# Kernel optimization log

Measured on AMD Instinct MI355X. Metric: run time of the kernel, lower is better.

The kernel has to match this reference:

```python
import jax, jax.numpy as jnp
import numpy as np
from jax import lax

EPS = 1e-5
TAU = 2.0
THR = 1.0

@jax.custom_vjp
def spike_fn(x):
    # torch.heaviside(x, 1.0): 1 where x >= 0, else 0
    return (x >= 0).astype(x.dtype)

def _spike_fwd(x):
    return spike_fn(x), x

def _spike_bwd(x, g):
    alpha = 4.0
    s = jax.nn.sigmoid(alpha * x)
    return (g * (1.0 - s) * s * alpha,)

spike_fn.defvjp(_spike_fwd, _spike_bwd)

def lif(x):
    # sequential membrane recurrence over dim 0 (time)
    def step(v, xt):
        v = v + (xt - v) / TAU
        s = spike_fn(v - THR)
        v = (1.0 - lax.stop_gradient(s)) * v
        return v, s
    _, spikes = lax.scan(step, jnp.zeros_like(x[0]), x)
    return spikes

def bn(x, p):
    # eval-mode BatchNorm2d; p = [weight, bias, mean, var], each [C]
    w, b, m, v = p
    inv = w / jnp.sqrt(v + EPS)
    return (x - m[None, :, None, None]) * inv[None, :, None, None] + b[None, :, None, None]

def bn_and_pad(x, p):
    # BN then pad 1 pixel on all sides with the BN-of-zero value
    w, b, m, v = p
    y = bn(x, p)
    pad_val = b - m * w / jnp.sqrt(v + EPS)  # [C]
    y = jnp.pad(y, ((0, 0), (0, 0), (1, 1), (1, 1)))
    pv = pad_val[None, :, None]  # broadcasts over batch and spatial
    y = y.at[:, :, 0, :].set(pv)
    y = y.at[:, :, -1, :].set(pv)
    y = y.at[:, :, :, 0].set(pv)
    y = y.at[:, :, :, -1].set(pv)
    return y

def branch(x, w1, dw, pw, bn3):
    # RepConv: 1x1 -> BNAndPad(1) -> depthwise3x3(valid) -> 1x1 -> BN, then outer BN
    C = x.shape[1]
    y = jnp.einsum('oc,bchw->bohw', w1, x)
    y = bn_and_pad(y, bn3[0])
    y = lax.conv_general_dilated(y, dw[:, None, :, :], (1, 1), 'VALID',
                                 dimension_numbers=('NCHW', 'OIHW', 'NCHW'),
                                 feature_group_count=C)
    y = jnp.einsum('oc,bchw->bohw', pw, y)
    y = bn(y, bn3[1])
    y = bn(y, bn3[2])
    return y

def _to_heads(t, B, N, h, d):
    # [B,C,H,W] -> [B,h,N,d]
    return t.reshape(B, h * d, N).transpose(0, 2, 1).reshape(B, N, h, d).transpose(0, 2, 1, 3)

def forward(x, q_w1, q_dw, q_pw, q_bn, k_w1, k_dw, k_pw, k_bn,
            v_w1, v_dw, v_pw, v_bn, p_w1, p_dw, p_pw, p_bn,
            num_heads=8):
    B, C, H, W = x.shape
    N = H * W
    h = num_heads
    d = C // h
    scale = float(d) ** -0.5

    xs = lif(x)
    q = lif(branch(xs, q_w1, q_dw, q_pw, q_bn))
    k = lif(branch(xs, k_w1, k_dw, k_pw, k_bn))
    v = lif(branch(xs, v_w1, v_dw, v_pw, v_bn))

    q = _to_heads(q, B, N, h, d)
    k = _to_heads(k, B, N, h, d)
    v = _to_heads(v, B, N, h, d)

    kv = jnp.einsum('bhnd,bhne->bhde', k, v)          # [B,h,d,d]
    o = jnp.einsum('bhnd,bhde->bhne', q, kv) * scale  # [B,h,N,d]
    o = o.transpose(0, 1, 3, 2).reshape(B, C, N)       # [B,C,N]
    o = lif(o)
    o = o.reshape(B, C, H, W)
    o = branch(o, p_w1, p_dw, p_pw, p_bn)
    return o.reshape(B, C, H, W)

def setup_inputs() -> dict:
    key = jax.random.key(0)
    ks = jax.random.split(key, 20)
    B, C, H, W = 8, 256, 64, 64
    s1 = 1.0 / np.sqrt(C)

    def make_bn(k):
        k1, k2, k3, k4 = jax.random.split(k, 4)
        w = 1.0 + 0.1 * jax.random.normal(k1, (3, C), jnp.float32)
        b = 0.1 * jax.random.normal(k2, (3, C), jnp.float32)
        m = 0.1 * jax.random.normal(k3, (3, C), jnp.float32)
        var = jax.random.uniform(k4, (3, C), jnp.float32, 0.5, 1.5)
        return jnp.stack([w, b, m, var], axis=1)  # [3,4,C]

    inp = {'x': jax.random.normal(ks[0], (B, C, H, W), jnp.float32)}
    for i, p in enumerate(['q', 'k', 'v', 'p']):
        kk = jax.random.split(ks[1 + i], 4)
        inp[p + '_w1'] = jax.random.normal(kk[0], (C, C), jnp.float32) * s1
        inp[p + '_dw'] = jax.random.normal(kk[1], (C, 3, 3), jnp.float32) * 0.3
        inp[p + '_pw'] = jax.random.normal(kk[2], (C, C), jnp.float32) * s1
        inp[p + '_bn'] = make_bn(kk[3])
    return inp

def reference(x, q_w1, q_dw, q_pw, q_bn, k_w1, k_dw, k_pw, k_bn,
              v_w1, v_dw, v_pw, v_bn, p_w1, p_dw, p_pw, p_bn):
    return forward(x, q_w1, q_dw, q_pw, q_bn, k_w1, k_dw, k_pw, k_bn,
                   v_w1, v_dw, v_pw, v_bn, p_w1, p_dw, p_pw, p_bn)
```

## Files before the change

kernel.cpp:

```cpp
#include <hip/hip_runtime.h>
#include <hip/hip_bf16.h>
#include <math.h>

#define T_ 8
#define C_ 256
#define N_ 4096
#define CN_ (C_ * N_)
#define EPSB 1e-5f

typedef unsigned long long u64;
typedef unsigned int u32;
typedef short bf16x8 __attribute__((ext_vector_type(8)));
typedef float f32x4 __attribute__((ext_vector_type(4)));

static __device__ __forceinline__ unsigned short f2bf(float f) {
    __hip_bfloat16 h = __float2bfloat16(f);
    return *(unsigned short*)&h;
}
static __device__ __forceinline__ float bf2f(unsigned short u) {
    u32 x = (u32)u << 16;
    return *(float*)&x;
}

typedef const __attribute__((address_space(1))) unsigned int ga_u32;
typedef __attribute__((address_space(3))) unsigned int la_u32;
static __device__ __forceinline__ void gl_lds16(const unsigned short* g,
                                                unsigned short* l_) {
    __builtin_amdgcn_global_load_lds((ga_u32*)g, (la_u32*)l_, 16, 0, 0);
}


__global__ __launch_bounds__(256) void lif_x_frag(const float* __restrict__ X,
                                                  unsigned short* __restrict__ ST) {
    int nb = blockIdx.x * 32;
    int c0 = blockIdx.y * 8;
    int tid = threadIdx.x;
    int nj = tid & 31, ci = tid >> 5;
    size_t base = (size_t)(c0 + ci) * N_ + nb + nj;
    __shared__ unsigned short Ls[8][34];
    int k32 = c0 >> 5, quad = (c0 >> 3) & 3;
    float v = 0.f;
#pragma unroll
    for (int t = 0; t < T_; t++) {
        float xt = X[(size_t)t * CN_ + base];
        v = v + (xt - v) / 2.0f;
        int s = (v - 1.0f >= 0.f) ? 1 : 0;
        Ls[ci][nj] = s ? (unsigned short)0x3F80 : (unsigned short)0;
        if (s) v = 0.f;
        __syncthreads();
        if (tid < 32) {
            int np = nb + tid;
            bf16x8 bs;
#pragma unroll
            for (int j = 0; j < 8; j++) bs[j] = (short)Ls[j][tid];
            *(bf16x8*)&ST[(size_t)t * CN_ +
                ((size_t)((np >> 4) * 8 + k32)) * 512 + (quad * 16 + (np & 15)) * 8] = bs;
        }
        __syncthreads();
    }
}

struct LArgs {
    const float* F[3];
    unsigned char* sq;
    u64* kbp;
    u64* vbp;
};
__global__ __launch_bounds__(256) void lif3(LArgs a) {
    int br = blockIdx.y;
    int idx = blockIdx.x * 256 + threadIdx.x;
    const float* X = a.F[br];
    int lane = threadIdx.x & 63;
    u64* BP = (br == 1) ? a.kbp : a.vbp;
    float v = 0.f;
#pragma unroll
    for (int t = 0; t < T_; t++) {
        float xt = X[(size_t)t * CN_ + idx];
        v = v + (xt - v) / 2.0f;
        int s = (v - 1.0f >= 0.f) ? 1 : 0;
        if (br == 0) {
            a.sq[(size_t)t * CN_ + idx] = (unsigned char)s;
        } else {
            u64 mask = __ballot(s);
            if (lane == 0) BP[((size_t)t * CN_ + idx) >> 6] = mask;
        }
        if (s) v = 0.f;
    }
}

struct WPtrs { const float* w[8]; };
__global__ __launch_bounds__(256) void split_w(WPtrs p, unsigned short* __restrict__ out) {
    int mat = blockIdx.y;
    int idx = blockIdx.x * 256 + threadIdx.x;
    int m = idx >> 8, k = idx & 255;
    float w = p.w[mat][idx];
    unsigned short h1 = f2bf(w);
    float f1 = bf2f(h1);
    unsigned short h2 = f2bf(w - f1);
    unsigned short h3 = f2bf(w - f1 - bf2f(h2));
    int lane = ((k >> 3) & 3) * 16 + (m & 15);
    size_t pos = ((size_t)(((m >> 4) * 8 + (k >> 5)) * 64 + lane)) * 8 + (k & 7);
    size_t base = (size_t)mat * 3 * 65536;
    out[base + pos] = h1;
    out[base + 65536 + pos] = h2;
    out[base + 2 * 65536 + pos] = h3;
}

static __device__ __forceinline__ void dw_body(const float* __restrict__ Yt,
                                               const float* __restrict__ dw,
                                               const float* __restrict__ bnp,
                                               unsigned short* __restrict__ Bh,
                                               unsigned short* __restrict__ Bl,
                                               int y0, int cg, int tid) {
    int c0 = cg * 8;
    __shared__ float L[8][6][68];
    __shared__ float invs[8], bs_[8], ms_[8], pads_[8];

    if (tid < 8) {
        int c = c0 + tid;
        float w = bnp[c], b = bnp[256 + c], m = bnp[512 + c], var = bnp[768 + c];
        float sq = sqrtf(var + EPSB);
        invs[tid] = w / sq;
        bs_[tid] = b;
        ms_[tid] = m;
        pads_[tid] = b - (m * w) / sq;
    }
    __syncthreads();

    for (int i = tid; i < 8 * 6 * 66; i += 256) {
        int c = i / 396;
        int rem = i - c * 396;
        int row = rem / 66, col = rem - row * 66;
        int gy = y0 - 1 + row, gx = col - 1;
        float val;
        if (gy < 0 || gy > 63 || gx < 0 || gx > 63) val = pads_[c];
        else val = (Yt[(size_t)(c0 + c) * N_ + gy * 64 + gx] - ms_[c]) * invs[c] + bs_[c];
        L[c][row][col] = val;
    }
    __syncthreads();

    int x = tid & 63, ry = tid >> 6;
    int n = (y0 + ry) * 64 + x;

    bf16x8 hi, lo;
#pragma unroll
    for (int j = 0; j < 8; j++) {
        const float* dwc = dw + (c0 + j) * 9;
        float a = 0.f;
#pragma unroll
        for (int dy = 0; dy < 3; dy++)
#pragma unroll
            for (int dx = 0; dx < 3; dx++)
                a += dwc[dy * 3 + dx] * L[j][ry + dy][x + dx];
        unsigned short h = f2bf(a);
        hi[j] = (short)h;
        lo[j] = (short)f2bf(a - bf2f(h));
    }
    size_t pos = ((size_t)((n >> 4) * 8 + (cg >> 2))) * 512 +
                 (size_t)(((cg & 3) * 16 + (n & 15)) * 8);
    *(bf16x8*)&Bh[pos] = hi;
    *(bf16x8*)&Bl[pos] = lo;
}

__global__ __launch_bounds__(256) void dw_bn_split(const float* __restrict__ Yin,
                                                   const float* __restrict__ dw,
                                                   const float* __restrict__ bnp,
                                                   unsigned short* __restrict__ BhT,
                                                   unsigned short* __restrict__ BlT) {
    int t = blockIdx.z;
    dw_body(Yin + (size_t)t * CN_, dw, bnp,
            BhT + (size_t)t * CN_, BlT + (size_t)t * CN_,
            blockIdx.x * 4, blockIdx.y, threadIdx.x);
}

struct DArgs {
    const float* F[3];
    const float* dw[3];
    const float* bn[3];
    unsigned short* Ph[3];
    unsigned short* Pl[3];
};
__global__ __launch_bounds__(256) void dw3(DArgs a) {
    int br = blockIdx.z >> 3, t = blockIdx.z & 7;
    dw_body(a.F[br] + (size_t)t * CN_, a.dw[br], a.bn[br],
            a.Ph[br] + (size_t)t * CN_, a.Pl[br] + (size_t)t * CN_,
            blockIdx.x * 4, blockIdx.y, threadIdx.x);
}

static __device__ __forceinline__ void gemm_s_core(const unsigned short* __restrict__ Wsp,
                                                   const unsigned short* __restrict__ Bt,
                                                   float* __restrict__ Yt,
                                                   int bx, int by, int tid) {
    int l = tid & 63, wave = tid >> 6;
    int wm = wave >> 1, wn = wave & 1;
    int lcol = l & 15, quad = l >> 4;

    __shared__ unsigned short As[24][512];
    __shared__ unsigned short Bs[8][512];

    f32x4 acc[4][4];
#pragma unroll
    for (int i = 0; i < 4; i++)
#pragma unroll
        for (int j = 0; j < 4; j++) acc[i][j] = (f32x4){0.f, 0.f, 0.f, 0.f};

    for (int k32 = 0; k32 < 8; k32++) {
#pragma unroll
        for (int i = 0; i < 8; i++) {
            int tau = wave * 8 + i;
            if (tau < 24) {
                int s = tau >> 3, mtg = tau & 7;
                gl_lds16(&Wsp[(size_t)s * 65536 +
                              ((size_t)((by * 8 + mtg) * 8 + k32)) * 512 + l * 8],
                         &As[tau][0]);
            } else {
                int nt = tau - 24;
                gl_lds16(&Bt[((size_t)((bx * 8 + nt) * 8 + k32)) * 512 + l * 8],
                         &Bs[nt][0]);
            }
        }
        __syncthreads();

        bf16x8 bfr[4];
#pragma unroll
        for (int nt = 0; nt < 4; nt++)
            bfr[nt] = *(const bf16x8*)&Bs[wn * 4 + nt][l * 8];
#pragma unroll
        for (int s = 0; s < 3; s++) {
#pragma unroll
            for (int mt = 0; mt < 4; mt++) {
                bf16x8 afr = *(const bf16x8*)&As[s * 8 + wm * 4 + mt][l * 8];
#pragma unroll
                for (int nt = 0; nt < 4; nt++)
                    acc[mt][nt] = __builtin_amdgcn_mfma_f32_16x16x32_bf16(
                        afr, bfr[nt], acc[mt][nt], 0, 0, 0);
            }
        }
        __syncthreads();
    }

    int m0 = by * 128, n0 = bx * 128;
#pragma unroll
    for (int mt = 0; mt < 4; mt++)
#pragma unroll
        for (int i = 0; i < 4; i++) {
            int row = m0 + wm * 64 + mt * 16 + quad * 4 + i;
            float* yr = &Yt[(size_t)row * N_ + n0 + wn * 64 + lcol];
#pragma unroll
            for (int nt = 0; nt < 4; nt++) yr[nt * 16] = acc[mt][nt][i];
        }
}

static __device__ __forceinline__ void gemm_f_core(const unsigned short* __restrict__ Wsp,
                                                   const unsigned short* __restrict__ Bht,
                                                   const unsigned short* __restrict__ Blt,
                                                   float* __restrict__ Yt,
                                                   const float* __restrict__ bnp,
                                                   int bx, int by, int tid) {
    int l = tid & 63, wave = tid >> 6;
    int wm = wave >> 1, wn = wave & 1;
    int lcol = l & 15, quad = l >> 4;

    __shared__ unsigned short As[24][512];
    __shared__ unsigned short Bhs[8][512];
    __shared__ unsigned short Bls[8][512];

    f32x4 acc[4][4];
#pragma unroll
    for (int i = 0; i < 4; i++)
#pragma unroll
        for (int j = 0; j < 4; j++) acc[i][j] = (f32x4){0.f, 0.f, 0.f, 0.f};

    for (int k32 = 0; k32 < 8; k32++) {
#pragma unroll
        for (int i = 0; i < 10; i++) {
            int tau = wave * 10 + i;
            if (tau < 24) {
                int s = tau >> 3, mtg = tau & 7;
                gl_lds16(&Wsp[(size_t)s * 65536 +
                              ((size_t)((by * 8 + mtg) * 8 + k32)) * 512 + l * 8],
                         &As[tau][0]);
            } else if (tau < 32) {
                int nt = tau - 24;
                gl_lds16(&Bht[((size_t)((bx * 8 + nt) * 8 + k32)) * 512 + l * 8],
                         &Bhs[nt][0]);
            } else {
                int nt = tau - 32;
                gl_lds16(&Blt[((size_t)((bx * 8 + nt) * 8 + k32)) * 512 + l * 8],
                         &Bls[nt][0]);
            }
        }
        __syncthreads();

        bf16x8 bh[4], bl[4];
#pragma unroll
        for (int nt = 0; nt < 4; nt++) {
            bh[nt] = *(const bf16x8*)&Bhs[wn * 4 + nt][l * 8];
            bl[nt] = *(const bf16x8*)&Bls[wn * 4 + nt][l * 8];
        }
#pragma unroll
        for (int s = 0; s < 3; s++) {
#pragma unroll
            for (int mt = 0; mt < 4; mt++) {
                bf16x8 afr = *(const bf16x8*)&As[s * 8 + wm * 4 + mt][l * 8];
#pragma unroll
                for (int nt = 0; nt < 4; nt++)
                    acc[mt][nt] = __builtin_amdgcn_mfma_f32_16x16x32_bf16(
                        afr, bh[nt], acc[mt][nt], 0, 0, 0);
                if (s < 2) {
#pragma unroll
                    for (int nt = 0; nt < 4; nt++)
                        acc[mt][nt] = __builtin_amdgcn_mfma_f32_16x16x32_bf16(
                            afr, bl[nt], acc[mt][nt], 0, 0, 0);
                }
            }
        }
        __syncthreads();
    }

    int m0 = by * 128, n0 = bx * 128;
#pragma unroll
    for (int mt = 0; mt < 4; mt++)
#pragma unroll
        for (int i = 0; i < 4; i++) {
            int row = m0 + wm * 64 + mt * 16 + quad * 4 + i;
            float i1 = bnp[1024 + row] / sqrtf(bnp[1024 + 768 + row] + EPSB);
            float b1 = bnp[1024 + 256 + row], m1 = bnp[1024 + 512 + row];
            float i2 = bnp[2048 + row] / sqrtf(bnp[2048 + 768 + row] + EPSB);
            float b2 = bnp[2048 + 256 + row], m2 = bnp[2048 + 512 + row];
            float* yr = &Yt[(size_t)row * N_ + n0 + wn * 64 + lcol];
#pragma unroll
            for (int nt = 0; nt < 4; nt++)
                yr[nt * 16] = ((acc[mt][nt][i] - m1) * i1 + b1 - m2) * i2 + b2;
        }
}

__global__ __launch_bounds__(256) void gemm_s2(const unsigned short* __restrict__ Wsp,
                                               const unsigned short* __restrict__ ST,
                                               float* __restrict__ Y) {
    int t = blockIdx.z;
    gemm_s_core(Wsp, ST + (size_t)t * CN_, Y + (size_t)t * CN_,
                blockIdx.x, blockIdx.y, threadIdx.x);
}
__global__ __launch_bounds__(256) void gemm_f2(const unsigned short* __restrict__ Wsp,
                                               const unsigned short* __restrict__ BhT,
                                               const unsigned short* __restrict__ BlT,
                                               float* __restrict__ Y,
                                               const float* __restrict__ bnp) {
    int t = blockIdx.z;
    gemm_f_core(Wsp, BhT + (size_t)t * CN_, BlT + (size_t)t * CN_,
                Y + (size_t)t * CN_, bnp, blockIdx.x, blockIdx.y, threadIdx.x);
}

struct GSArgs { const unsigned short* W[3]; const unsigned short* ST; float* F[3]; };
__global__ __launch_bounds__(256) void gemm_s3(GSArgs a) {
    int t = blockIdx.z;
    int br = blockIdx.y >> 1, byl = blockIdx.y & 1;
    gemm_s_core(a.W[br], a.ST + (size_t)t * CN_, a.F[br] + (size_t)t * CN_,
                blockIdx.x, byl, threadIdx.x);
}
struct GFArgs {
    const unsigned short* W[3];
    const unsigned short* Ph[3];
    const unsigned short* Pl[3];
    float* F[3];
    const float* bn[3];
};
__global__ __launch_bounds__(256) void gemm_f3(GFArgs a) {
    int t = blockIdx.z;
    int br = blockIdx.y >> 1, byl = blockIdx.y & 1;
    gemm_f_core(a.W[br], a.Ph[br] + (size_t)t * CN_, a.Pl[br] + (size_t)t * CN_,
                a.F[br] + (size_t)t * CN_, a.bn[br], blockIdx.x, byl, threadIdx.x);
}

__global__ __launch_bounds__(1024) void attn_kv_bp(const u64* __restrict__ Kbp,
                                                   const u64* __restrict__ Vbp,
                                                   float* __restrict__ kvbuf) {
    int th = blockIdx.x;
    int t = th >> 3, h = th & 7;
    const u64* kb = Kbp + ((size_t)t * C_ + h * 32) * 64;
    const u64* vb = Vbp + ((size_t)t * C_ + h * 32) * 64;
    __shared__ u64 ks[32][65];
    __shared__ u64 vs[32][65];
    int tid = threadIdx.x;
    {
        int r = tid >> 5, w2 = (tid & 31) * 2;
        ks[r][w2] = kb[r * 64 + w2];     ks[r][w2 + 1] = kb[r * 64 + w2 + 1];
        vs[r][w2] = vb[r * 64 + w2];     vs[r][w2 + 1] = vb[r * 64 + w2 + 1];
    }
    __syncthreads();
    int d = tid >> 5, e = tid & 31;
    int cnt = 0;
#pragma unroll
    for (int w = 0; w < 64; w++)
        cnt += __popcll(ks[d][w] & vs[e][w]);
    kvbuf[(size_t)th * 1024 + d * 32 + e] = (float)cnt;
}

__global__ __launch_bounds__(256) void attn_olif(const unsigned char* __restrict__ q,
                                                 const float* __restrict__ kvbuf,
                                                 unsigned short* __restrict__ ST) {
    int h = blockIdx.y;
    int nb = blockIdx.x * 128;
    int tid = threadIdx.x;
    int nj = tid & 127, eh = tid >> 7;
    int n = nb + nj;
    __shared__ float kvs[1024];
    const float scale = 0.17677669529663687f;
    float v[16];
#pragma unroll
    for (int e = 0; e < 16; e++) v[e] = 0.f;
    size_t posbase = ((size_t)((n >> 4) * 8 + h)) * 512 + (size_t)(n & 15) * 8;
    int quad0 = 2 * eh;
#pragma unroll
    for (int t = 0; t < T_; t++) {
        for (int i = tid; i < 1024; i += 256)
            kvs[i] = kvbuf[(size_t)(t * 8 + h) * 1024 + i];
        __syncthreads();
        float acc[16];
#pragma unroll
        for (int e = 0; e < 16; e++) acc[e] = 0.f;
        const unsigned char* qb = q + (size_t)t * CN_ + (size_t)(h * 32) * N_ + n;
#pragma unroll 4
        for (int d = 0; d < 32; d++) {
            float qd = (float)qb[(size_t)d * N_];
#pragma unroll
            for (int e = 0; e < 16; e++)
                acc[e] += qd * kvs[d * 32 + eh * 16 + e];
        }
        bf16x8 w0, w1;
#pragma unroll
        for (int e = 0; e < 16; e++) {
            float o = acc[e] * scale;
            v[e] = v[e] + (o - v[e]) / 2.0f;
            int s = (v[e] - 1.0f >= 0.f) ? 1 : 0;
            short bits = s ? (short)0x3F80 : (short)0;
            if (e < 8) w0[e] = bits; else w1[e - 8] = bits;
            if (s) v[e] = 0.f;
        }
        unsigned short* Stt = ST + (size_t)t * CN_;
        *(bf16x8*)&Stt[posbase + (size_t)(quad0 * 16) * 8] = w0;
        *(bf16x8*)&Stt[posbase + (size_t)((quad0 + 1) * 16) * 8] = w1;
        __syncthreads();
    }
}

extern "C" void kernel_launch(void* const* d_in, const int* in_sizes, int n_in,
                              void* d_out, int out_size, void* d_ws, size_t ws_size,
                              hipStream_t stream) {
    const float* x = (const float*)d_in[0];
    const float* q_w1 = (const float*)d_in[1];
    const float* q_dw = (const float*)d_in[2];
    const float* q_pw = (const float*)d_in[3];
    const float* q_bn = (const float*)d_in[4];
    const float* k_w1 = (const float*)d_in[5];
    const float* k_dw = (const float*)d_in[6];
    const float* k_pw = (const float*)d_in[7];
    const float* k_bn = (const float*)d_in[8];
    const float* v_w1 = (const float*)d_in[9];
    const float* v_dw = (const float*)d_in[10];
    const float* v_pw = (const float*)d_in[11];
    const float* v_bn = (const float*)d_in[12];
    const float* p_w1 = (const float*)d_in[13];
    const float* p_dw = (const float*)d_in[14];
    const float* p_pw = (const float*)d_in[15];
    const float* p_bn = (const float*)d_in[16];

    const size_t SZ = (size_t)T_ * CN_;
    float* out = (float*)d_out;
    float* F0 = (float*)d_ws;
    float* F1 = F0 + SZ;
    float* F2 = F1 + SZ;
    float* P0 = F2 + SZ;
    float* P1 = P0 + SZ;
    float* P2 = P1 + SZ;
    float* bufKV = P2 + SZ;
    unsigned char* xs = (unsigned char*)(bufKV + 65536);
    unsigned char* sq = xs + SZ;
    u64* kbp = (u64*)(sq + SZ);
    u64* vbp = kbp + (SZ >> 6);
    unsigned short* wspA = (unsigned short*)(vbp + (SZ >> 6));
    unsigned short* ST = wspA + 8 * 3 * 65536;

    unsigned short* P0h = (unsigned short*)P0; unsigned short* P0l = P0h + SZ;
    unsigned short* P1h = (unsigned short*)P1; unsigned short* P1l = P1h + SZ;
    unsigned short* P2h = (unsigned short*)P2; unsigned short* P2l = P2h + SZ;

    WPtrs wp;
    wp.w[0] = q_w1; wp.w[1] = q_pw; wp.w[2] = k_w1; wp.w[3] = k_pw;
    wp.w[4] = v_w1; wp.w[5] = v_pw; wp.w[6] = p_w1; wp.w[7] = p_pw;
    split_w<<<dim3(256, 8), dim3(256), 0, stream>>>(wp, wspA);
    const size_t WS3 = 3 * 65536;

    lif_x_frag<<<dim3(N_ / 32, C_ / 8), dim3(256), 0, stream>>>(x, ST);

    GSArgs gs;
    gs.W[0] = wspA + 0 * WS3; gs.W[1] = wspA + 2 * WS3; gs.W[2] = wspA + 4 * WS3;
    gs.ST = ST; gs.F[0] = F0; gs.F[1] = F1; gs.F[2] = F2;
    gemm_s3<<<dim3(N_ / 128, 6, T_), dim3(256), 0, stream>>>(gs);

    DArgs da;
    da.F[0] = F0; da.F[1] = F1; da.F[2] = F2;
    da.dw[0] = q_dw; da.dw[1] = k_dw; da.dw[2] = v_dw;
    da.bn[0] = q_bn; da.bn[1] = k_bn; da.bn[2] = v_bn;
    da.Ph[0] = P0h; da.Ph[1] = P1h; da.Ph[2] = P2h;
    da.Pl[0] = P0l; da.Pl[1] = P1l; da.Pl[2] = P2l;
    dw3<<<dim3(16, 32, 3 * T_), dim3(256), 0, stream>>>(da);

    GFArgs gf;
    gf.W[0] = wspA + 1 * WS3; gf.W[1] = wspA + 3 * WS3; gf.W[2] = wspA + 5 * WS3;
    gf.Ph[0] = P0h; gf.Ph[1] = P1h; gf.Ph[2] = P2h;
    gf.Pl[0] = P0l; gf.Pl[1] = P1l; gf.Pl[2] = P2l;
    gf.F[0] = F0; gf.F[1] = F1; gf.F[2] = F2;
    gf.bn[0] = q_bn; gf.bn[1] = k_bn; gf.bn[2] = v_bn;
    gemm_f3<<<dim3(N_ / 128, 6, T_), dim3(256), 0, stream>>>(gf);

    LArgs la;
    la.F[0] = F0; la.F[1] = F1; la.F[2] = F2;
    la.sq = sq; la.kbp = kbp; la.vbp = vbp;
    lif3<<<dim3(CN_ / 256, 3), dim3(256), 0, stream>>>(la);

    attn_kv_bp<<<dim3(64), dim3(1024), 0, stream>>>(kbp, vbp, bufKV);
    attn_olif<<<dim3(N_ / 128, 8), dim3(256), 0, stream>>>(sq, bufKV, ST);

    gemm_s2<<<dim3(N_ / 128, C_ / 128, T_), dim3(256), 0, stream>>>(wspA + 6 * WS3, ST, out);
    dw_bn_split<<<dim3(16, 32, T_), dim3(256), 0, stream>>>(out, p_dw, p_bn, P0h, P0l);
    gemm_f2<<<dim3(N_ / 128, C_ / 128, T_), dim3(256), 0, stream>>>(wspA + 7 * WS3, P0h, P0l, out, p_bn);
}
```

Baseline: 417.1 us.

## Double-buffer GEMM tiles with staged prefetch and 8-wave 128x256 blocks

Rewrites the split-precision bf16 GEMM cores to use 512-thread blocks covering a 128x256 output tile and double-buffered LDS. Loads for the next k-step are issued in stages, interleaved with MFMA phases, and gated by explicit vmcnt waits plus barriers. MFMA sections also raise wave priority. The aim is to hide global-to-LDS latency that the old load-sync-compute-sync loop exposed and to halve B-operand reuse cost per block. In exchange LDS use roughly doubles and the hand-tuned vmcnt counts must match the number of outstanding loads exactly.

Result: slower. 457.6 us (+9.7%).

```diff
diff --git a/kernel.cpp b/kernel.cpp
--- a/kernel.cpp
+++ b/kernel.cpp
@@ -187,16 +187,20 @@
             blockIdx.x * 4, blockIdx.y, threadIdx.x);
 }
 
-static __device__ __forceinline__ void gemm_s_core(const unsigned short* __restrict__ Wsp,
-                                                   const unsigned short* __restrict__ Bt,
-                                                   float* __restrict__ Yt,
-                                                   int bx, int by, int tid) {
+#define VMCNT_BAR(n) asm volatile("s_waitcnt vmcnt(" #n ")\ns_barrier" ::: "memory")
+
+static __device__ __forceinline__ void gemm_s_core8(const unsigned short* __restrict__ Wsp,
+                                                    const unsigned short* __restrict__ Bt,
+                                                    float* __restrict__ Yt,
+                                                    int bx, int Mh, int tid) {
     int l = tid & 63, wave = tid >> 6;
-    int wm = wave >> 1, wn = wave & 1;
+    int wm = wave >> 2, wn = wave & 3;
     int lcol = l & 15, quad = l >> 4;
 
-    __shared__ unsigned short As[24][512];
-    __shared__ unsigned short Bs[8][512];
+    __shared__ unsigned short A0[2][8][512];
+    __shared__ unsigned short A1[2][8][512];
+    __shared__ unsigned short A2[2][8][512];
+    __shared__ unsigned short BS[2][16][512];
 
     f32x4 acc[4][4];
 #pragma unroll
@@ -204,42 +208,83 @@
 #pragma unroll
         for (int j = 0; j < 4; j++) acc[i][j] = (f32x4){0.f, 0.f, 0.f, 0.f};
 
-    for (int k32 = 0; k32 < 8; k32++) {
-#pragma unroll
-        for (int i = 0; i < 8; i++) {
-            int tau = wave * 8 + i;
-            if (tau < 24) {
-                int s = tau >> 3, mtg = tau & 7;
-                gl_lds16(&Wsp[(size_t)s * 65536 +
-                              ((size_t)((by * 8 + mtg) * 8 + k32)) * 512 + l * 8],
-                         &As[tau][0]);
-            } else {
-                int nt = tau - 24;
-                gl_lds16(&Bt[((size_t)((bx * 8 + nt) * 8 + k32)) * 512 + l * 8],
-                         &Bs[nt][0]);
-            }
-        }
-        __syncthreads();
-
-        bf16x8 bfr[4];
-#pragma unroll
-        for (int nt = 0; nt < 4; nt++)
-            bfr[nt] = *(const bf16x8*)&Bs[wn * 4 + nt][l * 8];
-#pragma unroll
-        for (int s = 0; s < 3; s++) {
-#pragma unroll
-            for (int mt = 0; mt < 4; mt++) {
-                bf16x8 afr = *(const bf16x8*)&As[s * 8 + wm * 4 + mt][l * 8];
-#pragma unroll
-                for (int nt = 0; nt < 4; nt++)
-                    acc[mt][nt] = __builtin_amdgcn_mfma_f32_16x16x32_bf16(
-                        afr, bfr[nt], acc[mt][nt], 0, 0, 0);
-            }
-        }
-        __syncthreads();
-    }
-
-    int m0 = by * 128, n0 = bx * 128;
+    const int wA = wave * 3;
+
+    auto stg1 = [&](int k, int q) {
+#pragma unroll
+        for (int i = 0; i < 3; i++) {
+            int idx = wA + i;
+            if (idx < 16)
+                gl_lds16(&Bt[((size_t)(bx * 16 + idx) * 8 + k) * 512 + l * 8],
+                         &BS[q][idx][0]);
+            else
+                gl_lds16(&Wsp[((size_t)(Mh * 8 + (idx - 16)) * 8 + k) * 512 + l * 8],
+                         &A0[q][idx - 16][0]);
+        }
+    };
+    auto stg2 = [&](int k, int q) {
+        gl_lds16(&Wsp[65536 + ((size_t)(Mh * 8 + wave) * 8 + k) * 512 + l * 8],
+                 &A1[q][wave][0]);
+    };
+    auto stg3 = [&](int k, int q) {
+        gl_lds16(&Wsp[2 * 65536 + ((size_t)(Mh * 8 + wave) * 8 + k) * 512 + l * 8],
+                 &A2[q][wave][0]);
+    };
+
+    stg1(0, 0); stg2(0, 0); stg3(0, 0);
+
+    bf16x8 b[4], a[4];
+    for (int k = 0; k < 8; k++) {
+        int p = k & 1, q = p ^ 1;
+        int kn = (k < 7) ? k + 1 : 7;
+
+        stg1(kn, q);
+        VMCNT_BAR(5);
+#pragma unroll
+        for (int nt = 0; nt < 4; nt++) b[nt] = *(const bf16x8*)&BS[p][wn * 4 + nt][l * 8];
+#pragma unroll
+        for (int mt = 0; mt < 4; mt++) a[mt] = *(const bf16x8*)&A0[p][wm * 4 + mt][l * 8];
+        __builtin_amdgcn_s_setprio(1);
+#pragma unroll
+        for (int mt = 0; mt < 4; mt++)
+#pragma unroll
+            for (int nt = 0; nt < 4; nt++)
+                acc[mt][nt] = __builtin_amdgcn_mfma_f32_16x16x32_bf16(
+                    a[mt], b[nt], acc[mt][nt], 0, 0, 0);
+        __builtin_amdgcn_s_setprio(0);
+        __builtin_amdgcn_s_barrier();
+
+        stg2(kn, q);
+        VMCNT_BAR(5);
+#pragma unroll
+        for (int mt = 0; mt < 4; mt++) a[mt] = *(const bf16x8*)&A1[p][wm * 4 + mt][l * 8];
+        __builtin_amdgcn_s_setprio(1);
+#pragma unroll
+        for (int mt = 0; mt < 4; mt++)
+#pragma unroll
+            for (int nt = 0; nt < 4; nt++)
+                acc[mt][nt] = __builtin_amdgcn_mfma_f32_16x16x32_bf16(
+                    a[mt], b[nt], acc[mt][nt], 0, 0, 0);
+        __builtin_amdgcn_s_setprio(0);
+        __builtin_amdgcn_s_barrier();
+
+        stg3(kn, q);
+        VMCNT_BAR(5);
+#pragma unroll
+        for (int mt = 0; mt < 4; mt++) a[mt] = *(const bf16x8*)&A2[p][wm * 4 + mt][l * 8];
+        __builtin_amdgcn_s_setprio(1);
+#pragma unroll
+        for (int mt = 0; mt < 4; mt++)
+#pragma unroll
+            for (int nt = 0; nt < 4; nt++)
+                acc[mt][nt] = __builtin_amdgcn_mfma_f32_16x16x32_bf16(
+                    a[mt], b[nt], acc[mt][nt], 0, 0, 0);
+        __builtin_amdgcn_s_setprio(0);
+        __builtin_amdgcn_s_barrier();
+    }
+    asm volatile("s_waitcnt vmcnt(0)" ::: "memory");
+
+    int m0 = Mh * 128, n0 = bx * 256;
 #pragma unroll
     for (int mt = 0; mt < 4; mt++)
 #pragma unroll
@@ -251,19 +296,21 @@
         }
 }
 
-static __device__ __forceinline__ void gemm_f_core(const unsigned short* __restrict__ Wsp,
-                                                   const unsigned short* __restrict__ Bht,
-                                                   const unsigned short* __restrict__ Blt,
-                                                   float* __restrict__ Yt,
-                                                   const float* __restrict__ bnp,
-                                                   int bx, int by, int tid) {
+static __device__ __forceinline__ void gemm_f_core8(const unsigned short* __restrict__ Wsp,
+                                                    const unsigned short* __restrict__ Bht,
+                                                    const unsigned short* __restrict__ Blt,
+                                                    float* __restrict__ Yt,
+                                                    const float* __restrict__ bnp,
+                                                    int bx, int Mh, int tid) {
     int l = tid & 63, wave = tid >> 6;
-    int wm = wave >> 1, wn = wave & 1;
+    int wm = wave >> 2, wn = wave & 3;
     int lcol = l & 15, quad = l >> 4;
 
-    __shared__ unsigned short As[24][512];
-    __shared__ unsigned short Bhs[8][512];
-    __shared__ unsigned short Bls[8][512];
+    __shared__ unsigned short A0[2][8][512];
+    __shared__ unsigned short A1[2][8][512];
+    __shared__ unsigned short A2[2][8][512];
+    __shared__ unsigned short BH[2][16][512];
+    __shared__ unsigned short BL[2][16][512];
 
     f32x4 acc[4][4];
 #pragma unroll
@@ -271,54 +318,116 @@
 #pragma unroll
         for (int j = 0; j < 4; j++) acc[i][j] = (f32x4){0.f, 0.f, 0.f, 0.f};
 
-    for (int k32 = 0; k32 < 8; k32++) {
-#pragma unroll
-        for (int i = 0; i < 10; i++) {
-            int tau = wave * 10 + i;
-            if (tau < 24) {
-                int s = tau >> 3, mtg = tau & 7;
-                gl_lds16(&Wsp[(size_t)s * 65536 +
-                              ((size_t)((by * 8 + mtg) * 8 + k32)) * 512 + l * 8],
-                         &As[tau][0]);
-            } else if (tau < 32) {
-                int nt = tau - 24;
-                gl_lds16(&Bht[((size_t)((bx * 8 + nt) * 8 + k32)) * 512 + l * 8],
-                         &Bhs[nt][0]);
-            } else {
-                int nt = tau - 32;
-                gl_lds16(&Blt[((size_t)((bx * 8 + nt) * 8 + k32)) * 512 + l * 8],
-                         &Bls[nt][0]);
-            }
-        }
-        __syncthreads();
-
-        bf16x8 bh[4], bl[4];
-#pragma unroll
-        for (int nt = 0; nt < 4; nt++) {
-            bh[nt] = *(const bf16x8*)&Bhs[wn * 4 + nt][l * 8];
-            bl[nt] = *(const bf16x8*)&Bls[wn * 4 + nt][l * 8];
-        }
-#pragma unroll
-        for (int s = 0; s < 3; s++) {
-#pragma unroll
-            for (int mt = 0; mt < 4; mt++) {
-                bf16x8 afr = *(const bf16x8*)&As[s * 8 + wm * 4 + mt][l * 8];
-#pragma unroll
-                for (int nt = 0; nt < 4; nt++)
-                    acc[mt][nt] = __builtin_amdgcn_mfma_f32_16x16x32_bf16(
-                        afr, bh[nt], acc[mt][nt], 0, 0, 0);
-                if (s < 2) {
-#pragma unroll
-                    for (int nt = 0; nt < 4; nt++)
-                        acc[mt][nt] = __builtin_amdgcn_mfma_f32_16x16x32_bf16(
-                            afr, bl[nt], acc[mt][nt], 0, 0, 0);
-                }
-            }
-        }
-        __syncthreads();
-    }
-
-    int m0 = by * 128, n0 = bx * 128;
+    const int wA = wave * 3;
+    const int wB = wave * 2;
+
+    auto stgA = [&](int k, int q) {
+#pragma unroll
+        for (int i = 0; i < 3; i++) {
+            int idx = wA + i;
+            if (idx < 16)
+                gl_lds16(&Bht[((size_t)(bx * 16 + idx) * 8 + k) * 512 + l * 8],
+                         &BH[q][idx][0]);
+            else
+                gl_lds16(&Wsp[((size_t)(Mh * 8 + (idx - 16)) * 8 + k) * 512 + l * 8],
+                         &A0[q][idx - 16][0]);
+        }
+    };
+    auto stgB = [&](int k, int q) {
+#pragma unroll
+        for (int i = 0; i < 2; i++) {
+            int idx = wB + i;
+            gl_lds16(&Blt[((size_t)(bx * 16 + idx) * 8 + k) * 512 + l * 8],
+                     &BL[q][idx][0]);
+        }
+    };
+    auto stgC = [&](int k, int q) {
+        gl_lds16(&Wsp[65536 + ((size_t)(Mh * 8 + wave) * 8 + k) * 512 + l * 8],
+                 &A1[q][wave][0]);
+    };
+    auto stgE = [&](int k, int q) {
+        gl_lds16(&Wsp[2 * 65536 + ((size_t)(Mh * 8 + wave) * 8 + k) * 512 + l * 8],
+                 &A2[q][wave][0]);
+    };
+
+    stgA(0, 0); stgB(0, 0); stgC(0, 0); stgE(0, 0);
+
+    bf16x8 bh[4], bl[4], a[4];
+    for (int k = 0; k < 8; k++) {
+        int p = k & 1, q = p ^ 1;
+        int kn = (k < 7) ? k + 1 : 7;
+
+        stgA(kn, q);
+        VMCNT_BAR(7);
+#pragma unroll
+        for (int nt = 0; nt < 4; nt++) bh[nt] = *(const bf16x8*)&BH[p][wn * 4 + nt][l * 8];
+#pragma unroll
+        for (int mt = 0; mt < 4; mt++) a[mt] = *(const bf16x8*)&A0[p][wm * 4 + mt][l * 8];
+        __builtin_amdgcn_s_setprio(1);
+#pragma unroll
+        for (int mt = 0; mt < 4; mt++)
+#pragma unroll
+            for (int nt = 0; nt < 4; nt++)
+                acc[mt][nt] = __builtin_amdgcn_mfma_f32_16x16x32_bf16(
+                    a[mt], bh[nt], acc[mt][nt], 0, 0, 0);
+        __builtin_amdgcn_s_setprio(0);
+        __builtin_amdgcn_s_barrier();
+
+        stgB(kn, q);
+        VMCNT_BAR(7);
+#pragma unroll
+        for (int nt = 0; nt < 4; nt++) bl[nt] = *(const bf16x8*)&BL[p][wn * 4 + nt][l * 8];
+        __builtin_amdgcn_s_setprio(1);
+#pragma unroll
+        for (int mt = 0; mt < 4; mt++)
+#pragma unroll
+            for (int nt = 0; nt < 4; nt++)
+                acc[mt][nt] = __builtin_amdgcn_mfma_f32_16x16x32_bf16(
+                    a[mt], bl[nt], acc[mt][nt], 0, 0, 0);
+        __builtin_amdgcn_s_setprio(0);
+        __builtin_amdgcn_s_barrier();
+
+        stgC(kn, q);
+        VMCNT_BAR(7);
+#pragma unroll
+        for (int mt = 0; mt < 4; mt++) a[mt] = *(const bf16x8*)&A1[p][wm * 4 + mt][l * 8];
+        __builtin_amdgcn_s_setprio(1);
+#pragma unroll
+        for (int mt = 0; mt < 4; mt++)
+#pragma unroll
+            for (int nt = 0; nt < 4; nt++)
+                acc[mt][nt] = __builtin_amdgcn_mfma_f32_16x16x32_bf16(
+                    a[mt], bh[nt], acc[mt][nt], 0, 0, 0);
+        __builtin_amdgcn_s_setprio(0);
+        __builtin_amdgcn_s_barrier();
+
+        __builtin_amdgcn_s_setprio(1);
+#pragma unroll
+        for (int mt = 0; mt < 4; mt++)
+#pragma unroll
+            for (int nt = 0; nt < 4; nt++)
+                acc[mt][nt] = __builtin_amdgcn_mfma_f32_16x16x32_bf16(
+                    a[mt], bl[nt], acc[mt][nt], 0, 0, 0);
+        __builtin_amdgcn_s_setprio(0);
+        __builtin_amdgcn_s_barrier();
+
+        stgE(kn, q);
+        VMCNT_BAR(7);
+#pragma unroll
+        for (int mt = 0; mt < 4; mt++) a[mt] = *(const bf16x8*)&A2[p][wm * 4 + mt][l * 8];
+        __builtin_amdgcn_s_setprio(1);
+#pragma unroll
+        for (int mt = 0; mt < 4; mt++)
+#pragma unroll
+            for (int nt = 0; nt < 4; nt++)
+                acc[mt][nt] = __builtin_amdgcn_mfma_f32_16x16x32_bf16(
+                    a[mt], bh[nt], acc[mt][nt], 0, 0, 0);
+        __builtin_amdgcn_s_setprio(0);
+        __builtin_amdgcn_s_barrier();
+    }
+    asm volatile("s_waitcnt vmcnt(0)" ::: "memory");
+
+    int m0 = Mh * 128, n0 = bx * 256;
 #pragma unroll
     for (int mt = 0; mt < 4; mt++)
 #pragma unroll
@@ -326,38 +435,38 @@
             int row = m0 + wm * 64 + mt * 16 + quad * 4 + i;
             float i1 = bnp[1024 + row] / sqrtf(bnp[1024 + 768 + row] + EPSB);
             float b1 = bnp[1024 + 256 + row], m1 = bnp[1024 + 512 + row];
-            float i2 = bnp[2048 + row] / sqrtf(bnp[2048 + 768 + row] + EPSB);
+            float i2v = bnp[2048 + row] / sqrtf(bnp[2048 + 768 + row] + EPSB);
             float b2 = bnp[2048 + 256 + row], m2 = bnp[2048 + 512 + row];
             float* yr = &Yt[(size_t)row * N_ + n0 + wn * 64 + lcol];
 #pragma unroll
             for (int nt = 0; nt < 4; nt++)
-                yr[nt * 16] = ((acc[mt][nt][i] - m1) * i1 + b1 - m2) * i2 + b2;
-        }
-}
-
-__global__ __launch_bounds__(256) void gemm_s2(const unsigned short* __restrict__ Wsp,
+                yr[nt * 16] = ((acc[mt][nt][i] - m1) * i1 + b1 - m2) * i2v + b2;
+        }
+}
+
+__global__ __launch_bounds__(512) void gemm_s2(const unsigned short* __restrict__ Wsp,
                                                const unsigned short* __restrict__ ST,
                                                float* __restrict__ Y) {
     int t = blockIdx.z;
-    gemm_s_core(Wsp, ST + (size_t)t * CN_, Y + (size_t)t * CN_,
-                blockIdx.x, blockIdx.y, threadIdx.x);
-}
-__global__ __launch_bounds__(256) void gemm_f2(const unsigned short* __restrict__ Wsp,
+    gemm_s_core8(Wsp, ST + (size_t)t * CN_, Y + (size_t)t * CN_,
+                 blockIdx.x, blockIdx.y, threadIdx.x);
+}
+__global__ __launch_bounds__(512) void gemm_f2(const unsigned short* __restrict__ Wsp,
                                                const unsigned short* __restrict__ BhT,
                                                const unsigned short* __restrict__ BlT,
                                                float* __restrict__ Y,
                                                const float* __restrict__ bnp) {
     int t = blockIdx.z;
-    gemm_f_core(Wsp, BhT + (size_t)t * CN_, BlT + (size_t)t * CN_,
-                Y + (size_t)t * CN_, bnp, blockIdx.x, blockIdx.y, threadIdx.x);
+    gemm_f_core8(Wsp, BhT + (size_t)t * CN_, BlT + (size_t)t * CN_,
+                 Y + (size_t)t * CN_, bnp, blockIdx.x, blockIdx.y, threadIdx.x);
 }
 
 struct GSArgs { const unsigned short* W[3]; const unsigned short* ST; float* F[3]; };
-__global__ __launch_bounds__(256) void gemm_s3(GSArgs a) {
+__global__ __launch_bounds__(512) void gemm_s3(GSArgs a) {
     int t = blockIdx.z;
-    int br = blockIdx.y >> 1, byl = blockIdx.y & 1;
-    gemm_s_core(a.W[br], a.ST + (size_t)t * CN_, a.F[br] + (size_t)t * CN_,
-                blockIdx.x, byl, threadIdx.x);
+    int br = blockIdx.y >> 1, Mh = blockIdx.y & 1;
+    gemm_s_core8(a.W[br], a.ST + (size_t)t * CN_, a.F[br] + (size_t)t * CN_,
+                 blockIdx.x, Mh, threadIdx.x);
 }
 struct GFArgs {
     const unsigned short* W[3];
@@ -366,11 +475,11 @@
     float* F[3];
     const float* bn[3];
 };
-__global__ __launch_bounds__(256) void gemm_f3(GFArgs a) {
+__global__ __launch_bounds__(512) void gemm_f3(GFArgs a) {
     int t = blockIdx.z;
-    int br = blockIdx.y >> 1, byl = blockIdx.y & 1;
-    gemm_f_core(a.W[br], a.Ph[br] + (size_t)t * CN_, a.Pl[br] + (size_t)t * CN_,
-                a.F[br] + (size_t)t * CN_, a.bn[br], blockIdx.x, byl, threadIdx.x);
+    int br = blockIdx.y >> 1, Mh = blockIdx.y & 1;
+    gemm_f_core8(a.W[br], a.Ph[br] + (size_t)t * CN_, a.Pl[br] + (size_t)t * CN_,
+                 a.F[br] + (size_t)t * CN_, a.bn[br], blockIdx.x, Mh, threadIdx.x);
 }
 
 __global__ __launch_bounds__(1024) void attn_kv_bp(const u64* __restrict__ Kbp,
@@ -497,7 +606,7 @@
     GSArgs gs;
     gs.W[0] = wspA + 0 * WS3; gs.W[1] = wspA + 2 * WS3; gs.W[2] = wspA + 4 * WS3;
     gs.ST = ST; gs.F[0] = F0; gs.F[1] = F1; gs.F[2] = F2;
-    gemm_s3<<<dim3(N_ / 128, 6, T_), dim3(256), 0, stream>>>(gs);
+    gemm_s3<<<dim3(N_ / 256, 6, T_), dim3(512), 0, stream>>>(gs);
 
     DArgs da;
     da.F[0] = F0; da.F[1] = F1; da.F[2] = F2;
@@ -513,7 +622,7 @@
     gf.Pl[0] = P0l; gf.Pl[1] = P1l; gf.Pl[2] = P2l;
     gf.F[0] = F0; gf.F[1] = F1; gf.F[2] = F2;
     gf.bn[0] = q_bn; gf.bn[1] = k_bn; gf.bn[2] = v_bn;
-    gemm_f3<<<dim3(N_ / 128, 6, T_), dim3(256), 0, stream>>>(gf);
+    gemm_f3<<<dim3(N_ / 256, 6, T_), dim3(512), 0, stream>>>(gf);
 
     LArgs la;
     la.F[0] = F0; la.F[1] = F1; la.F[2] = F2;
@@ -523,7 +632,7 @@
     attn_kv_bp<<<dim3(64), dim3(1024), 0, stream>>>(kbp, vbp, bufKV);
     attn_olif<<<dim3(N_ / 128, 8), dim3(256), 0, stream>>>(sq, bufKV, ST);
 
-    gemm_s2<<<dim3(N_ / 128, C_ / 128, T_), dim3(256), 0, stream>>>(wspA + 6 * WS3, ST, out);
+    gemm_s2<<<dim3(N_ / 256, C_ / 128, T_), dim3(512), 0, stream>>>(wspA + 6 * WS3, ST, out);
     dw_bn_split<<<dim3(16, 32, T_), dim3(256), 0, stream>>>(out, p_dw, p_bn, P0h, P0l);
-    gemm_f2<<<dim3(N_ / 128, C_ / 128, T_), dim3(256), 0, stream>>>(wspA + 7 * WS3, P0h, P0l, out, p_bn);
-}
+    gemm_f2<<<dim3(N_ / 256, C_ / 128, T_), dim3(512), 0, stream>>>(wspA + 7 * WS3, P0h, P0l, out, p_bn);
+}
```

## Double-buffer LDS tiles in split-bf16 GEMM cores to overlap loads with MFMA

Applied to the files above, without the earlier changes.

Both GEMM cores now keep two LDS buffers and issue the global-to-LDS loads for the next k-slice before running the MFMAs on the current one. Each iteration ends with one barrier that also drains outstanding vector memory ops, replacing the two syncthreads per iteration. This hides global load latency behind compute. In exchange LDS use doubles (about 64 KB for the f core), which can lower occupancy.

After: 412.3 us. No clear change (-1.2%).

```diff
diff --git a/kernel.cpp b/kernel.cpp
--- a/kernel.cpp
+++ b/kernel.cpp
@@ -28,6 +28,8 @@
                                                 unsigned short* l_) {
     __builtin_amdgcn_global_load_lds((ga_u32*)g, (la_u32*)l_, 16, 0, 0);
 }
+
+#define DRAIN_BAR() asm volatile("s_waitcnt vmcnt(0)\ns_barrier" ::: "memory")
 
 
 __global__ __launch_bounds__(256) void lif_x_frag(const float* __restrict__ X,
@@ -195,8 +197,8 @@
     int wm = wave >> 1, wn = wave & 1;
     int lcol = l & 15, quad = l >> 4;
 
-    __shared__ unsigned short As[24][512];
-    __shared__ unsigned short Bs[8][512];
+    __shared__ unsigned short As[2][24][512];
+    __shared__ unsigned short Bs[2][8][512];
 
     f32x4 acc[4][4];
 #pragma unroll
@@ -204,7 +206,7 @@
 #pragma unroll
         for (int j = 0; j < 4; j++) acc[i][j] = (f32x4){0.f, 0.f, 0.f, 0.f};
 
-    for (int k32 = 0; k32 < 8; k32++) {
+    auto stg = [&](int k32, int bq) {
 #pragma unroll
         for (int i = 0; i < 8; i++) {
             int tau = wave * 8 + i;
@@ -212,31 +214,38 @@
                 int s = tau >> 3, mtg = tau & 7;
                 gl_lds16(&Wsp[(size_t)s * 65536 +
                               ((size_t)((by * 8 + mtg) * 8 + k32)) * 512 + l * 8],
-                         &As[tau][0]);
+                         &As[bq][tau][0]);
             } else {
                 int nt = tau - 24;
                 gl_lds16(&Bt[((size_t)((bx * 8 + nt) * 8 + k32)) * 512 + l * 8],
-                         &Bs[nt][0]);
+                         &Bs[bq][nt][0]);
             }
         }
-        __syncthreads();
+    };
+
+    stg(0, 0);
+    DRAIN_BAR();
+
+    for (int k32 = 0; k32 < 8; k32++) {
+        int p = k32 & 1;
+        if (k32 < 7) stg(k32 + 1, p ^ 1);
 
         bf16x8 bfr[4];
 #pragma unroll
         for (int nt = 0; nt < 4; nt++)
-            bfr[nt] = *(const bf16x8*)&Bs[wn * 4 + nt][l * 8];
+            bfr[nt] = *(const bf16x8*)&Bs[p][wn * 4 + nt][l * 8];
 #pragma unroll
         for (int s = 0; s < 3; s++) {
 #pragma unroll
             for (int mt = 0; mt < 4; mt++) {
-                bf16x8 afr = *(const bf16x8*)&As[s * 8 + wm * 4 + mt][l * 8];
+                bf16x8 afr = *(const bf16x8*)&As[p][s * 8 + wm * 4 + mt][l * 8];
 #pragma unroll
                 for (int nt = 0; nt < 4; nt++)
                     acc[mt][nt] = __builtin_amdgcn_mfma_f32_16x16x32_bf16(
                         afr, bfr[nt], acc[mt][nt], 0, 0, 0);
             }
         }
-        __syncthreads();
+        DRAIN_BAR();
     }
 
     int m0 = by * 128, n0 = bx * 128;
@@ -261,9 +270,9 @@
     int wm = wave >> 1, wn = wave & 1;
     int lcol = l & 15, quad = l >> 4;
 
-    __shared__ unsigned short As[24][512];
-    __shared__ unsigned short Bhs[8][512];
-    __shared__ unsigned short Bls[8][512];
+    __shared__ unsigned short As[2][24][512];
+    __shared__ unsigned short Bhs[2][8][512];
+    __shared__ unsigned short Bls[2][8][512];
 
     f32x4 acc[4][4];
 #pragma unroll
@@ -271,7 +280,7 @@
 #pragma unroll
         for (int j = 0; j < 4; j++) acc[i][j] = (f32x4){0.f, 0.f, 0.f, 0.f};
 
-    for (int k32 = 0; k32 < 8; k32++) {
+    auto stg = [&](int k32, int bq) {
 #pragma unroll
         for (int i = 0; i < 10; i++) {
             int tau = wave * 10 + i;
@@ -279,30 +288,37 @@
                 int s = tau >> 3, mtg = tau & 7;
                 gl_lds16(&Wsp[(size_t)s * 65536 +
                               ((size_t)((by * 8 + mtg) * 8 + k32)) * 512 + l * 8],
-                         &As[tau][0]);
+                         &As[bq][tau][0]);
             } else if (tau < 32) {
                 int nt = tau - 24;
                 gl_lds16(&Bht[((size_t)((bx * 8 + nt) * 8 + k32)) * 512 + l * 8],
-                         &Bhs[nt][0]);
+                         &Bhs[bq][nt][0]);
             } else {
                 int nt = tau - 32;
                 gl_lds16(&Blt[((size_t)((bx * 8 + nt) * 8 + k32)) * 512 + l * 8],
-                         &Bls[nt][0]);
+                         &Bls[bq][nt][0]);
             }
         }
-        __syncthreads();
+    };
+
+    stg(0, 0);
+    DRAIN_BAR();
+
+    for (int k32 = 0; k32 < 8; k32++) {
+        int p = k32 & 1;
+        if (k32 < 7) stg(k32 + 1, p ^ 1);
 
         bf16x8 bh[4], bl[4];
 #pragma unroll
         for (int nt = 0; nt < 4; nt++) {
-            bh[nt] = *(const bf16x8*)&Bhs[wn * 4 + nt][l * 8];
-            bl[nt] = *(const bf16x8*)&Bls[wn * 4 + nt][l * 8];
+            bh[nt] = *(const bf16x8*)&Bhs[p][wn * 4 + nt][l * 8];
+            bl[nt] = *(const bf16x8*)&Bls[p][wn * 4 + nt][l * 8];
         }
 #pragma unroll
         for (int s = 0; s < 3; s++) {
 #pragma unroll
             for (int mt = 0; mt < 4; mt++) {
-                bf16x8 afr = *(const bf16x8*)&As[s * 8 + wm * 4 + mt][l * 8];
+                bf16x8 afr = *(const bf16x8*)&As[p][s * 8 + wm * 4 + mt][l * 8];
 #pragma unroll
                 for (int nt = 0; nt < 4; nt++)
                     acc[mt][nt] = __builtin_amdgcn_mfma_f32_16x16x32_bf16(
@@ -315,7 +331,7 @@
                 }
             }
         }
-        __syncthreads();
+        DRAIN_BAR();
     }
 
     int m0 = by * 128, n0 = bx * 128;
```

## Load GEMM fragments directly from global into registers with double buffering

Applied to the files above, without the earlier changes.

The GEMM cores no longer stage weight and activation tiles through LDS with global_load_lds and block barriers. Each wave now loads its own MFMA fragments straight from global memory into registers and prefetches the next K-slice while the current one is multiplied. Launch bounds also request two blocks per CU. This removes the LDS round trip and the barriers, but data shared between waves is now fetched redundantly from global or L2, and the doubled register buffers raise register pressure.

Result: slower. 504.7 us (+21.0%).

```diff
diff --git a/kernel.cpp b/kernel.cpp
--- a/kernel.cpp
+++ b/kernel.cpp
@@ -20,13 +20,6 @@
 static __device__ __forceinline__ float bf2f(unsigned short u) {
     u32 x = (u32)u << 16;
     return *(float*)&x;
-}
-
-typedef const __attribute__((address_space(1))) unsigned int ga_u32;
-typedef __attribute__((address_space(3))) unsigned int la_u32;
-static __device__ __forceinline__ void gl_lds16(const unsigned short* g,
-                                                unsigned short* l_) {
-    __builtin_amdgcn_global_load_lds((ga_u32*)g, (la_u32*)l_, 16, 0, 0);
 }
 
 
@@ -191,12 +184,22 @@
                                                    const unsigned short* __restrict__ Bt,
                                                    float* __restrict__ Yt,
                                                    int bx, int by, int tid) {
-    int l = tid & 63, wave = tid >> 6;
+    int l = tid & 63;
+    int wave = __builtin_amdgcn_readfirstlane(tid >> 6);
     int wm = wave >> 1, wn = wave & 1;
     int lcol = l & 15, quad = l >> 4;
 
-    __shared__ unsigned short As[24][512];
-    __shared__ unsigned short Bs[8][512];
+    const unsigned short* aS[3][4];
+    const unsigned short* bS[4];
+#pragma unroll
+    for (int s = 0; s < 3; s++)
+#pragma unroll
+        for (int mt = 0; mt < 4; mt++)
+            aS[s][mt] = Wsp + (size_t)s * 65536 +
+                        ((size_t)((by * 8 + wm * 4 + mt) * 8)) * 512 + l * 8;
+#pragma unroll
+    for (int nt = 0; nt < 4; nt++)
+        bS[nt] = Bt + ((size_t)((bx * 8 + wn * 4 + nt) * 8)) * 512 + l * 8;
 
     f32x4 acc[4][4];
 #pragma unroll
@@ -204,39 +207,41 @@
 #pragma unroll
         for (int j = 0; j < 4; j++) acc[i][j] = (f32x4){0.f, 0.f, 0.f, 0.f};
 
-    for (int k32 = 0; k32 < 8; k32++) {
-#pragma unroll
-        for (int i = 0; i < 8; i++) {
-            int tau = wave * 8 + i;
-            if (tau < 24) {
-                int s = tau >> 3, mtg = tau & 7;
-                gl_lds16(&Wsp[(size_t)s * 65536 +
-                              ((size_t)((by * 8 + mtg) * 8 + k32)) * 512 + l * 8],
-                         &As[tau][0]);
-            } else {
-                int nt = tau - 24;
-                gl_lds16(&Bt[((size_t)((bx * 8 + nt) * 8 + k32)) * 512 + l * 8],
-                         &Bs[nt][0]);
-            }
-        }
-        __syncthreads();
-
-        bf16x8 bfr[4];
-#pragma unroll
-        for (int nt = 0; nt < 4; nt++)
-            bfr[nt] = *(const bf16x8*)&Bs[wn * 4 + nt][l * 8];
-#pragma unroll
-        for (int s = 0; s < 3; s++) {
+    bf16x8 ab[2][3][4], bb[2][4];
+
+#pragma unroll
+    for (int s = 0; s < 3; s++)
+#pragma unroll
+        for (int mt = 0; mt < 4; mt++)
+            ab[0][s][mt] = *(const bf16x8*)(aS[s][mt]);
+#pragma unroll
+    for (int nt = 0; nt < 4; nt++)
+        bb[0][nt] = *(const bf16x8*)(bS[nt]);
+
+#pragma unroll
+    for (int k = 0; k < 8; k++) {
+        const int cur = k & 1, nxt = cur ^ 1;
+        if (k < 7) {
+            const int off = (k + 1) * 512;
+#pragma unroll
+            for (int s = 0; s < 3; s++)
+#pragma unroll
+                for (int mt = 0; mt < 4; mt++)
+                    ab[nxt][s][mt] = *(const bf16x8*)(aS[s][mt] + off);
+#pragma unroll
+            for (int nt = 0; nt < 4; nt++)
+                bb[nxt][nt] = *(const bf16x8*)(bS[nt] + off);
+        }
+#pragma unroll
+        for (int s = 0; s < 3; s++)
 #pragma unroll
             for (int mt = 0; mt < 4; mt++) {
-                bf16x8 afr = *(const bf16x8*)&As[s * 8 + wm * 4 + mt][l * 8];
+                bf16x8 afr = ab[cur][s][mt];
 #pragma unroll
                 for (int nt = 0; nt < 4; nt++)
                     acc[mt][nt] = __builtin_amdgcn_mfma_f32_16x16x32_bf16(
-                        afr, bfr[nt], acc[mt][nt], 0, 0, 0);
+                        afr, bb[cur][nt], acc[mt][nt], 0, 0, 0);
             }
-        }
-        __syncthreads();
     }
 
     int m0 = by * 128, n0 = bx * 128;
@@ -257,13 +262,26 @@
                                                    float* __restrict__ Yt,
                                                    const float* __restrict__ bnp,
                                                    int bx, int by, int tid) {
-    int l = tid & 63, wave = tid >> 6;
+    int l = tid & 63;
+    int wave = __builtin_amdgcn_readfirstlane(tid >> 6);
     int wm = wave >> 1, wn = wave & 1;
     int lcol = l & 15, quad = l >> 4;
 
-    __shared__ unsigned short As[24][512];
-    __shared__ unsigned short Bhs[8][512];
-    __shared__ unsigned short Bls[8][512];
+    const unsigned short* aS[3][4];
+    const unsigned short* bhS[4];
+    const unsigned short* blS[4];
+#pragma unroll
+    for (int s = 0; s < 3; s++)
+#pragma unroll
+        for (int mt = 0; mt < 4; mt++)
+            aS[s][mt] = Wsp + (size_t)s * 65536 +
+                        ((size_t)((by * 8 + wm * 4 + mt) * 8)) * 512 + l * 8;
+#pragma unroll
+    for (int nt = 0; nt < 4; nt++) {
+        size_t boff = ((size_t)((bx * 8 + wn * 4 + nt) * 8)) * 512 + l * 8;
+        bhS[nt] = Bht + boff;
+        blS[nt] = Blt + boff;
+    }
 
     f32x4 acc[4][4];
 #pragma unroll
@@ -271,51 +289,51 @@
 #pragma unroll
         for (int j = 0; j < 4; j++) acc[i][j] = (f32x4){0.f, 0.f, 0.f, 0.f};
 
-    for (int k32 = 0; k32 < 8; k32++) {
-#pragma unroll
-        for (int i = 0; i < 10; i++) {
-            int tau = wave * 10 + i;
-            if (tau < 24) {
-                int s = tau >> 3, mtg = tau & 7;
-                gl_lds16(&Wsp[(size_t)s * 65536 +
-                              ((size_t)((by * 8 + mtg) * 8 + k32)) * 512 + l * 8],
-                         &As[tau][0]);
-            } else if (tau < 32) {
-                int nt = tau - 24;
-                gl_lds16(&Bht[((size_t)((bx * 8 + nt) * 8 + k32)) * 512 + l * 8],
-                         &Bhs[nt][0]);
-            } else {
-                int nt = tau - 32;
-                gl_lds16(&Blt[((size_t)((bx * 8 + nt) * 8 + k32)) * 512 + l * 8],
-                         &Bls[nt][0]);
+    bf16x8 ab[2][3][4], bhb[2][4], blb[2][4];
+
+#pragma unroll
+    for (int s = 0; s < 3; s++)
+#pragma unroll
+        for (int mt = 0; mt < 4; mt++)
+            ab[0][s][mt] = *(const bf16x8*)(aS[s][mt]);
+#pragma unroll
+    for (int nt = 0; nt < 4; nt++) {
+        bhb[0][nt] = *(const bf16x8*)(bhS[nt]);
+        blb[0][nt] = *(const bf16x8*)(blS[nt]);
+    }
+
+#pragma unroll
+    for (int k = 0; k < 8; k++) {
+        const int cur = k & 1, nxt = cur ^ 1;
+        if (k < 7) {
+            const int off = (k + 1) * 512;
+#pragma unroll
+            for (int s = 0; s < 3; s++)
+#pragma unroll
+                for (int mt = 0; mt < 4; mt++)
+                    ab[nxt][s][mt] = *(const bf16x8*)(aS[s][mt] + off);
+#pragma unroll
+            for (int nt = 0; nt < 4; nt++) {
+                bhb[nxt][nt] = *(const bf16x8*)(bhS[nt] + off);
+                blb[nxt][nt] = *(const bf16x8*)(blS[nt] + off);
             }
         }
-        __syncthreads();
-
-        bf16x8 bh[4], bl[4];
-#pragma unroll
-        for (int nt = 0; nt < 4; nt++) {
-            bh[nt] = *(const bf16x8*)&Bhs[wn * 4 + nt][l * 8];
-            bl[nt] = *(const bf16x8*)&Bls[wn * 4 + nt][l * 8];
-        }
-#pragma unroll
-        for (int s = 0; s < 3; s++) {
+#pragma unroll
+        for (int s = 0; s < 3; s++)
 #pragma unroll
             for (int mt = 0; mt < 4; mt++) {
-                bf16x8 afr = *(const bf16x8*)&As[s * 8 + wm * 4 + mt][l * 8];
+                bf16x8 afr = ab[cur][s][mt];
 #pragma unroll
                 for (int nt = 0; nt < 4; nt++)
                     acc[mt][nt] = __builtin_amdgcn_mfma_f32_16x16x32_bf16(
-                        afr, bh[nt], acc[mt][nt], 0, 0, 0);
+                        afr, bhb[cur][nt], acc[mt][nt], 0, 0, 0);
                 if (s < 2) {
 #pragma unroll
                     for (int nt = 0; nt < 4; nt++)
                         acc[mt][nt] = __builtin_amdgcn_mfma_f32_16x16x32_bf16(
-                            afr, bl[nt], acc[mt][nt], 0, 0, 0);
+                            afr, blb[cur][nt], acc[mt][nt], 0, 0, 0);
                 }
             }
-        }
-        __syncthreads();
     }
 
     int m0 = by * 128, n0 = bx * 128;
@@ -335,25 +353,25 @@
         }
 }
 
-__global__ __launch_bounds__(256) void gemm_s2(const unsigned short* __restrict__ Wsp,
-                                               const unsigned short* __restrict__ ST,
-                                               float* __restrict__ Y) {
+__global__ __launch_bounds__(256, 2) void gemm_s2(const unsigned short* __restrict__ Wsp,
+                                                  const unsigned short* __restrict__ ST,
+                                                  float* __restrict__ Y) {
     int t = blockIdx.z;
     gemm_s_core(Wsp, ST + (size_t)t * CN_, Y + (size_t)t * CN_,
                 blockIdx.x, blockIdx.y, threadIdx.x);
 }
-__global__ __launch_bounds__(256) void gemm_f2(const unsigned short* __restrict__ Wsp,
-                                               const unsigned short* __restrict__ BhT,
-                                               const unsigned short* __restrict__ BlT,
-                                               float* __restrict__ Y,
-                                               const float* __restrict__ bnp) {
+__global__ __launch_bounds__(256, 2) void gemm_f2(const unsigned short* __restrict__ Wsp,
+                                                  const unsigned short* __restrict__ BhT,
+                                                  const unsigned short* __restrict__ BlT,
+                                                  float* __restrict__ Y,
+                                                  const float* __restrict__ bnp) {
     int t = blockIdx.z;
     gemm_f_core(Wsp, BhT + (size_t)t * CN_, BlT + (size_t)t * CN_,
                 Y + (size_t)t * CN_, bnp, blockIdx.x, blockIdx.y, threadIdx.x);
 }
 
 struct GSArgs { const unsigned short* W[3]; const unsigned short* ST; float* F[3]; };
-__global__ __launch_bounds__(256) void gemm_s3(GSArgs a) {
+__global__ __launch_bounds__(256, 2) void gemm_s3(GSArgs a) {
     int t = blockIdx.z;
     int br = blockIdx.y >> 1, byl = blockIdx.y & 1;
     gemm_s_core(a.W[br], a.ST + (size_t)t * CN_, a.F[br] + (size_t)t * CN_,
@@ -366,7 +384,7 @@
     float* F[3];
     const float* bn[3];
 };
-__global__ __launch_bounds__(256) void gemm_f3(GFArgs a) {
+__global__ __launch_bounds__(256, 2) void gemm_f3(GFArgs a) {
     int t = blockIdx.z;
     int br = blockIdx.y >> 1, byl = blockIdx.y & 1;
     gemm_f_core(a.W[br], a.Ph[br] + (size_t)t * CN_, a.Pl[br] + (size_t)t * CN_,
```
